# Performance work log

Measured on AMD Instinct MI355X. Metric: run time of the kernel, lower is better.

The kernel has to match this reference:

```python
import jax, jax.numpy as jnp
import numpy as np
from jax import lax

DN = ('NHWC', 'HWIO', 'NHWC')  # conv dimension numbers


def setup_inputs() -> dict:
    key = jax.random.key(0)
    ks = jax.random.split(key, 10)
    B, H, W, C, F, E = 16, 32, 32, 128, 128, 8
    G = F * (H // 2) * (W // 2)  # 32768, gating flatten size
    return {
        'x': jax.random.normal(ks[0], (B, H, W, C), jnp.float32),
        'eps_kernel': jax.random.normal(ks[1], (3, 3, C, F, E), jnp.float32),
        'eps_gate': jax.random.normal(ks[2], (B, E), jnp.float32),
        'expert_mu': jax.random.normal(ks[3], (3, 3, C, F, E), jnp.float32) * 0.05,
        'expert_rho': jax.random.normal(ks[4], (3, C, F, E), jnp.float32) * 0.01 - 6.0,
        'expert_bias': jax.random.normal(ks[5], (F, E), jnp.float32) * 0.01,
        'gating_kernel': jax.random.normal(ks[6], (3, 3, C, F), jnp.float32) * 0.05,
        'gating_bias': jax.random.normal(ks[7], (F,), jnp.float32) * 0.01,
        'gating_out_kernel': jax.random.normal(ks[8], (G, E), jnp.float32) * 0.01,
        'gating_out_bias': jax.random.normal(ks[9], (E,), jnp.float32) * 0.01,
    }


def reference(x, eps_kernel, eps_gate, expert_mu, expert_rho, expert_bias,
              gating_kernel, gating_bias, gating_out_kernel, gating_out_bias):
    GATING_NOISE_SIGMA = 1e-4
    TOP_K = 2
    B = x.shape[0]
    kh, kw, C, F, E = expert_mu.shape

    # Bayesian reparameterized expert kernels: rho shared over first kernel dim
    sigma = jax.nn.softplus(expert_rho)[None]               # [1,kw,C,F,E]
    kernel = expert_mu + sigma * eps_kernel                 # [kh,kw,C,F,E]

    # All-expert conv as one grouped conv via output-channel packing
    kern_flat = kernel.reshape(kh, kw, C, F * E)
    expert_out = lax.conv_general_dilated(x, kern_flat, (1, 1), 'SAME',
                                          dimension_numbers=DN)
    expert_out = expert_out.reshape(B, x.shape[1], x.shape[2], F, E)
    expert_out = expert_out + expert_bias                   # [B,H,W,F,E]

    # Gating path: conv -> 2x2 maxpool -> flatten -> dense -> noisy logits
    g = lax.conv_general_dilated(x, gating_kernel, (1, 1), 'SAME',
                                 dimension_numbers=DN) + gating_bias
    g = lax.reduce_window(g, -jnp.inf, lax.max,
                          (1, 2, 2, 1), (1, 2, 2, 1), 'VALID')
    logits = g.reshape(B, -1) @ gating_out_kernel + gating_out_bias  # [B,E]
    logits = logits + GATING_NOISE_SIGMA * eps_gate

    # noisy top-k gating: softmax over selected experts, zero elsewhere
    top_vals, top_idx = lax.top_k(logits, TOP_K)
    top_w = jax.nn.softmax(top_vals, axis=-1)
    gates = jnp.zeros((B, E), logits.dtype).at[
        jnp.arange(B)[:, None], top_idx].set(top_w)

    # combine experts weighted by gates, broadcast over spatial dims
    out = jnp.einsum('bhwfe,be->bhwf', expert_out, gates)
    return out
```

## Files before the change

### kernel.cpp

```cpp
#include <hip/hip_runtime.h>
#include <cmath>

#define B_ 16
#define H_ 32
#define W_ 32
#define C_ 128
#define F_ 128
#define KSZ (9*C_*F_)
#define NKS 36
#define FRAG_ELE 4096

typedef __bf16 bf16;
typedef __bf16 bf16x4 __attribute__((ext_vector_type(4)));
typedef __bf16 bf16x8 __attribute__((ext_vector_type(8)));
typedef float  f32x4  __attribute__((ext_vector_type(4)));

__device__ __forceinline__ float softplus_f(float v) {
  return log1pf(expf(-fabsf(v))) + fmaxf(v, 0.f);
}

__device__ __forceinline__ float logit_f(const float* part, const float* gob,
                                         const float* epsg, int bb, int e) {
  float s = 0.f;
  #pragma unroll
  for (int hb = 0; hb < 16; ++hb) s += part[(bb*16 + hb)*8 + e];
  return s + gob[e] + 1e-4f * epsg[bb*8 + e];
}

__device__ __forceinline__ void block_map_f(int bid, int* b, int* hb) {
  *b  = (bid & 7) * 2 + (bid >> 7);
  *hb = (bid >> 3) & 15;
}

template<int MODE>
__global__ __launch_bounds__(1024) void conv_k(
    const float* __restrict__ x,
    const bf16* __restrict__ Bhi,
    const bf16* __restrict__ Blo,
    const float* __restrict__ gb,
    const float* __restrict__ Wg,
    const float* __restrict__ part,
    const float* __restrict__ gob,
    const float* __restrict__ epsg,
    const float* __restrict__ ebias,
    const float* __restrict__ mu,
    const float* __restrict__ rho,
    const float* __restrict__ epsk,
    bf16* __restrict__ bank,
    float* __restrict__ outv)
{
  const int t = threadIdx.x;
  const int l = t & 63;

  if (MODE == 2 && blockIdx.x < NKS) {
    if (t < 512) {
      const int ks = blockIdx.x;
      const int nf = t >> 6;
      const int khkw = ks >> 2, kw = khkw % 3;
      const int f  = nf*16 + (l & 15);
      const int cb = (ks & 3)*32 + (l >> 4)*8;
      bf16x8 ob[8];
      #pragma unroll
      for (int j = 0; j < 8; ++j) {
        const int c = cb + j;
        const float* mp = &mu  [(size_t)((khkw*C_ + c)*F_ + f) * 8];
        const float* ep = &epsk[(size_t)((khkw*C_ + c)*F_ + f) * 8];
        const float* rp = &rho [(size_t)((kw  *C_ + c)*F_ + f) * 8];
        #pragma unroll
        for (int e = 0; e < 8; ++e)
          ob[e][j] = (bf16)(mp[e] + softplus_f(rp[e]) * ep[e]);
      }
      #pragma unroll
      for (int e = 0; e < 8; ++e) {
        size_t o = (size_t)e*KSZ + (size_t)ks*FRAG_ELE + nf*512 + l*8;
        *(bf16x8*)&bank[o] = ob[e];
      }
    }
    return;
  }

  int b, hb;
  block_map_f(MODE == 2 ? blockIdx.x - NKS : blockIdx.x, &b, &hb);
  const int wid = t >> 6;
  const int kg  = wid >> 3;
  const int w8  = wid & 7;

  __shared__ bf16 xs[MODE*4*34*128];
  __shared__ float red[8][8];
  __shared__ float gl8[8];
  __shared__ float gw2[2];
  __shared__ int   eid2[2];

  for (int v = t; v < 4*34*32; v += 1024) {
    int c4   = v & 31;
    int col  = (v >> 5) % 34;
    int rowi = (v >> 5) / 34;
    int row  = hb*2 - 1 + rowi;
    int w    = col - 1;
    float4 xv = make_float4(0.f, 0.f, 0.f, 0.f);
    if (row >= 0 && row < H_ && w >= 0 && w < W_)
      xv = *(const float4*)&x[((b*H_ + row)*W_ + w)*C_ + c4*4];
    float vv[4] = {xv.x, xv.y, xv.z, xv.w};
    bf16x4 h4, l4;
    #pragma unroll
    for (int j = 0; j < 4; ++j) {
      h4[j] = (bf16)vv[j];
      if (MODE == 2) l4[j] = (bf16)(vv[j] - (float)h4[j]);
    }
    int base = ((rowi*34 + col)*256 + c4*8) ^ ((col & 7) << 4);
    *(bf16x4*)((char*)xs + base) = h4;
    if (MODE == 2) *(bf16x4*)((char*)xs + 34816 + base) = l4;
  }
  if (MODE == 1 && t == 0) {
    float lg[8];
    #pragma unroll
    for (int e = 0; e < 8; ++e) lg[e] = logit_f(part, gob, epsg, b, e);
    int i0 = 0;
    #pragma unroll
    for (int e = 1; e < 8; ++e) if (lg[e] > lg[i0]) i0 = e;
    int i1 = (i0 == 0) ? 1 : 0;
    #pragma unroll
    for (int e = 0; e < 8; ++e) if (e != i0 && lg[e] > lg[i1]) i1 = e;
    float m  = fmaxf(lg[i0], lg[i1]);
    float e0 = expf(lg[i0] - m), e1 = expf(lg[i1] - m);
    float s  = e0 + e1;
    #pragma unroll
    for (int e = 0; e < 8; ++e) gl8[e] = 0.f;
    gl8[i0] = e0 / s;  gl8[i1] = e1 / s;
    eid2[0] = i0;      eid2[1] = i1;
    gw2[0]  = e0 / s;  gw2[1]  = e1 / s;
  }
  __syncthreads();

  const int mpar = w8 & 1;
  const int nf0  = (w8 >> 1) << 1;
  const int r15  = l & 15;
  const int q    = l >> 4;

  f32x4 acc00 = {0.f,0.f,0.f,0.f}, acc01 = acc00, acc10 = acc00, acc11 = acc00;
  f32x4 acd00 = acc00, acd01 = acc00, acd10 = acc00, acd11 = acc00;

  const bf16* B0;
  const bf16* B1;
  if (MODE == 1) { B0 = Bhi + (size_t)eid2[0]*KSZ; B1 = Bhi + (size_t)eid2[1]*KSZ; }
  else           { B0 = Bhi;                       B1 = Blo; }
  const size_t bgo = (size_t)(nf0*512 + l*8);

  bf16x8 s0h0,s0h1,s0l0,s0l1, s1h0,s1h1,s1l0,s1l1, s2h0,s2h1,s2l0,s2l1;

#define LOADB(S, KS_) do {                                                  \
    int kk_ = (KS_); if (kk_ > NKS-1) kk_ = NKS-1;                          \
    size_t o_ = bgo + (size_t)kk_ * FRAG_ELE;                               \
    S##h0 = *(const bf16x8*)(B0 + o_);                                      \
    S##h1 = *(const bf16x8*)(B0 + o_ + 512);                                \
    S##l0 = *(const bf16x8*)(B1 + o_);                                      \
    S##l1 = *(const bf16x8*)(B1 + o_ + 512);                                \
  } while (0)

#define MFMA16(a, bb_, c) __builtin_amdgcn_mfma_f32_16x16x32_bf16(a, bb_, c, 0, 0, 0)

#define COMPUTE(S, KS_) do {                                                \
    const int khkw_ = (KS_) >> 2;                                           \
    const int kh_ = khkw_ / 3, kw_ = khkw_ % 3;                             \
    const int c0_ = ((KS_) & 3) << 5;                                       \
    const int col_ = mpar*16 + r15 + kw_;                                   \
    const int off_ = ((kh_*34 + col_)*256 + (c0_ + q*8)*2) ^ ((col_ & 7) << 4); \
    bf16x8 a0_ = *(const bf16x8*)((const char*)xs + off_);                  \
    bf16x8 a1_ = *(const bf16x8*)((const char*)xs + off_ + 8704);           \
    __builtin_amdgcn_s_setprio(1);                                          \
    acc00 = MFMA16(a0_, S##h0, acc00);                                      \
    acc01 = MFMA16(a0_, S##h1, acc01);                                      \
    acc10 = MFMA16(a1_, S##h0, acc10);                                      \
    acc11 = MFMA16(a1_, S##h1, acc11);                                      \
    if (MODE == 2) {                                                        \
      bf16x8 g0_ = *(const bf16x8*)((const char*)xs + 34816 + off_);        \
      bf16x8 g1_ = *(const bf16x8*)((const char*)xs + 34816 + off_ + 8704); \
      acc00 = MFMA16(g0_, S##h0, acc00);                                    \
      acc01 = MFMA16(g0_, S##h1, acc01);                                    \
      acc10 = MFMA16(g1_, S##h0, acc10);                                    \
      acc11 = MFMA16(g1_, S##h1, acc11);                                    \
      acc00 = MFMA16(a0_, S##l0, acc00);                                    \
      acc01 = MFMA16(a0_, S##l1, acc01);                                    \
      acc10 = MFMA16(a1_, S##l0, acc10);                                    \
      acc11 = MFMA16(a1_, S##l1, acc11);                                    \
    } else {                                                                \
      acd00 = MFMA16(a0_, S##l0, acd00);                                    \
      acd01 = MFMA16(a0_, S##l1, acd01);                                    \
      acd10 = MFMA16(a1_, S##l0, acd10);                                    \
      acd11 = MFMA16(a1_, S##l1, acd11);                                    \
    }                                                                       \
    __builtin_amdgcn_s_setprio(0);                                          \
  } while (0)

  const int ks0 = kg * (NKS/2);
  LOADB(s0, ks0); LOADB(s1, ks0+1); LOADB(s2, ks0+2);
  for (int ks = ks0; ks < ks0 + NKS/2; ks += 3) {
    COMPUTE(s0, ks);   LOADB(s0, ks+3);
    COMPUTE(s1, ks+1); LOADB(s1, ks+4);
    COMPUTE(s2, ks+2); LOADB(s2, ks+5);
  }
#undef LOADB
#undef COMPUTE

  if (MODE == 1) {
    const float g0 = gw2[0], g1 = gw2[1];
    #pragma unroll
    for (int r = 0; r < 4; ++r) {
      acc00[r] = g0*acc00[r] + g1*acd00[r];
      acc01[r] = g0*acc01[r] + g1*acd01[r];
      acc10[r] = g0*acc10[r] + g1*acd10[r];
      acc11[r] = g0*acc11[r] + g1*acd11[r];
    }
  }

  __syncthreads();
  float* comb = (float*)xs;
  if (kg == 1) {
    #pragma unroll
    for (int r = 0; r < 4; ++r) {
      comb[(w8*16 + 0  + r)*64 + l] = acc00[r];
      comb[(w8*16 + 4  + r)*64 + l] = acc01[r];
      comb[(w8*16 + 8  + r)*64 + l] = acc10[r];
      comb[(w8*16 + 12 + r)*64 + l] = acc11[r];
    }
  }
  __syncthreads();
  if (kg == 0) {
    #pragma unroll
    for (int r = 0; r < 4; ++r) {
      acc00[r] += comb[(w8*16 + 0  + r)*64 + l];
      acc01[r] += comb[(w8*16 + 4  + r)*64 + l];
      acc10[r] += comb[(w8*16 + 8  + r)*64 + l];
      acc11[r] += comb[(w8*16 + 12 + r)*64 + l];
    }
  }

  if (MODE == 1) {
    if (kg == 0) {
      const int f0 = nf0*16 + r15;
      float bv0 = 0.f, bv1 = 0.f;
      #pragma unroll
      for (int e = 0; e < 8; ++e) {
        bv0 += gl8[e] * ebias[f0*8 + e];
        bv1 += gl8[e] * ebias[(f0+16)*8 + e];
      }
      #pragma unroll
      for (int mi = 0; mi < 2; ++mi) {
        const int h = hb*2 + mi;
        #pragma unroll
        for (int r = 0; r < 4; ++r) {
          const int wo = mpar*16 + q*4 + r;
          float* o = &outv[((b*H_ + h)*W_ + wo)*F_];
          o[f0]      = (mi ? acc10[r] : acc00[r]) + bv0;
          o[f0 + 16] = (mi ? acc11[r] : acc01[r]) + bv1;
        }
      }
    }
  } else {
    float pr[8] = {0,0,0,0,0,0,0,0};
    if (kg == 0) {
      #pragma unroll
      for (int ni = 0; ni < 2; ++ni) {
        const int f = (nf0 + ni)*16 + r15;
        const float bv = gb[f];
        #pragma unroll
        for (int pp = 0; pp < 2; ++pp) {
          float m0 = ni ? fmaxf(acc01[2*pp], acc01[2*pp+1])
                        : fmaxf(acc00[2*pp], acc00[2*pp+1]);
          float m1 = ni ? fmaxf(acc11[2*pp], acc11[2*pp+1])
                        : fmaxf(acc10[2*pp], acc10[2*pp+1]);
          float pm = fmaxf(m0, m1) + bv;
          const int pw = mpar*8 + q*2 + pp;
          const float* wr = &Wg[(size_t)((hb*16 + pw)*128 + f) * 8];
          float4 wA = *(const float4*)wr;
          float4 wB = *(const float4*)(wr + 4);
          pr[0] += pm*wA.x; pr[1] += pm*wA.y; pr[2] += pm*wA.z; pr[3] += pm*wA.w;
          pr[4] += pm*wB.x; pr[5] += pm*wB.y; pr[6] += pm*wB.z; pr[7] += pm*wB.w;
        }
      }
    }
    #pragma unroll
    for (int o = 32; o > 0; o >>= 1)
      #pragma unroll
      for (int e = 0; e < 8; ++e) pr[e] += __shfl_down(pr[e], o);
    if (l == 0 && kg == 0)
      #pragma unroll
      for (int e = 0; e < 8; ++e) red[w8][e] = pr[e];
    __syncthreads();
    if (t < 8) {
      float s = 0.f;
      #pragma unroll
      for (int w = 0; w < 8; ++w) s += red[w][t];
      outv[(b*16 + hb)*8 + t] = s;
    }
  }
}

__global__ __launch_bounds__(1024) void gkprep_k(
    const float* __restrict__ gk, bf16* __restrict__ bgh, bf16* __restrict__ bgl)
{
  __shared__ float tile[32*129];
  const int ks   = blockIdx.x;
  const int khkw = ks >> 2;
  const int cb   = (ks & 3)*32;
  const int t    = threadIdx.x;

  {
    int c  = t >> 5;
    int f4 = (t & 31) * 4;
    float4 val = *(const float4*)&gk[(size_t)(khkw*C_ + cb + c)*F_ + f4];
    float* dst = &tile[c*129 + f4];
    dst[0] = val.x; dst[1] = val.y; dst[2] = val.z; dst[3] = val.w;
  }
  __syncthreads();

  if (t < 512) {
    const int nf = t >> 6, l = t & 63;
    const int f  = nf*16 + (l & 15);
    bf16x8 h8, l8;
    #pragma unroll
    for (int j = 0; j < 8; ++j) {
      int c = (l >> 4)*8 + j;
      float v = tile[c*129 + f];
      bf16 h = (bf16)v;
      h8[j] = h;
      l8[j] = (bf16)(v - (float)h);
    }
    *(bf16x8*)&bgh[(size_t)ks*FRAG_ELE + t*8] = h8;
    *(bf16x8*)&bgl[(size_t)ks*FRAG_ELE + t*8] = l8;
  }
}

extern "C" void kernel_launch(void* const* d_in, const int* in_sizes, int n_in,
                              void* d_out, int out_size, void* d_ws, size_t ws_size,
                              hipStream_t stream) {
  const float* x    = (const float*)d_in[0];
  const float* epsk = (const float*)d_in[1];
  const float* epsg = (const float*)d_in[2];
  const float* mu   = (const float*)d_in[3];
  const float* rho  = (const float*)d_in[4];
  const float* ebias= (const float*)d_in[5];
  const float* gk   = (const float*)d_in[6];
  const float* gb   = (const float*)d_in[7];
  const float* gok  = (const float*)d_in[8];
  const float* gob  = (const float*)d_in[9];
  float* out = (float*)d_out;

  char* ws = (char*)d_ws;
  bf16*  bank = (bf16*) (ws);
  bf16*  bgh  = (bf16*) (ws + 2359296);
  bf16*  bgl  = (bf16*) (ws + 2654208);
  float* part = (float*)(ws + 2949120);

  gkprep_k<<<NKS, 1024, 0, stream>>>(gk, bgh, bgl);
  conv_k<2><<<NKS + 256, 1024, 0, stream>>>(x, bgh, bgl, gb, gok,
                                            nullptr, nullptr, nullptr, nullptr,
                                            mu, rho, epsk, bank, part);
  conv_k<1><<<256, 1024, 0, stream>>>(x, bank, nullptr, nullptr, nullptr,
                                      part, gob, epsg, ebias,
                                      nullptr, nullptr, nullptr, nullptr, out);
}
```

Measured before the change: 55.03 us.

## Pre-pad and pre-convert input to bf16 hi/lo, stage via global_load_lds

```diff
diff --git a/kernel.cpp b/kernel.cpp
--- a/kernel.cpp
+++ b/kernel.cpp
@@ -9,6 +9,7 @@
 #define KSZ (9*C_*F_)
 #define NKS 36
 #define FRAG_ELE 4096
+#define XPB (34*34*128)
 
 typedef __bf16 bf16;
 typedef __bf16 bf16x4 __attribute__((ext_vector_type(4)));
@@ -34,7 +35,7 @@
 
 template<int MODE>
 __global__ __launch_bounds__(1024) void conv_k(
-    const float* __restrict__ x,
+    const bf16* __restrict__ xpadh, const bf16* __restrict__ xpadl,
     const bf16* __restrict__ Bhi,
     const bf16* __restrict__ Blo,
     const float* __restrict__ gb,
@@ -91,26 +92,6 @@
   __shared__ float gw2[2];
   __shared__ int   eid2[2];
 
-  for (int v = t; v < 4*34*32; v += 1024) {
-    int c4   = v & 31;
-    int col  = (v >> 5) % 34;
-    int rowi = (v >> 5) / 34;
-    int row  = hb*2 - 1 + rowi;
-    int w    = col - 1;
-    float4 xv = make_float4(0.f, 0.f, 0.f, 0.f);
-    if (row >= 0 && row < H_ && w >= 0 && w < W_)
-      xv = *(const float4*)&x[((b*H_ + row)*W_ + w)*C_ + c4*4];
-    float vv[4] = {xv.x, xv.y, xv.z, xv.w};
-    bf16x4 h4, l4;
-    #pragma unroll
-    for (int j = 0; j < 4; ++j) {
-      h4[j] = (bf16)vv[j];
-      if (MODE == 2) l4[j] = (bf16)(vv[j] - (float)h4[j]);
-    }
-    int base = ((rowi*34 + col)*256 + c4*8) ^ ((col & 7) << 4);
-    *(bf16x4*)((char*)xs + base) = h4;
-    if (MODE == 2) *(bf16x4*)((char*)xs + 34816 + base) = l4;
-  }
   if (MODE == 1 && t == 0) {
     float lg[8];
     #pragma unroll
@@ -129,6 +110,26 @@
     gl8[i0] = e0 / s;  gl8[i1] = e1 / s;
     eid2[0] = i0;      eid2[1] = i1;
     gw2[0]  = e0 / s;  gw2[1]  = e1 / s;
+  }
+
+  {
+    const size_t bb = (size_t)b * XPB;
+    const int rowbase = hb * 2;
+    for (int dd = wid; dd < 34*MODE; dd += 16) {
+      const int variant = (MODE == 2 && dd >= 34) ? 1 : 0;
+      const int d = dd - 34*variant;
+      const int L = d*4 + (l >> 4);
+      const int rowi = L / 34;
+      const int col  = L % 34;
+      const int srcoff = ((l & 15)*16) ^ ((col & 7) << 4);
+      const bf16* src = (variant ? xpadl : xpadh) + bb
+                        + ((size_t)(rowbase + rowi)*34 + col)*128
+                        + (srcoff >> 1);
+      bf16* dst = &xs[variant*(4*34*128) + d*512];
+      __builtin_amdgcn_global_load_lds(
+          (const __attribute__((address_space(1))) void*)src,
+          (__attribute__((address_space(3))) void*)dst, 16, 0, 0);
+    }
   }
   __syncthreads();
 
@@ -167,7 +168,6 @@
     const int off_ = ((kh_*34 + col_)*256 + (c0_ + q*8)*2) ^ ((col_ & 7) << 4); \
     bf16x8 a0_ = *(const bf16x8*)((const char*)xs + off_);                  \
     bf16x8 a1_ = *(const bf16x8*)((const char*)xs + off_ + 8704);           \
-    __builtin_amdgcn_s_setprio(1);                                          \
     acc00 = MFMA16(a0_, S##h0, acc00);                                      \
     acc01 = MFMA16(a0_, S##h1, acc01);                                      \
     acc10 = MFMA16(a1_, S##h0, acc10);                                      \
@@ -189,7 +189,6 @@
       acd10 = MFMA16(a1_, S##l0, acd10);                                    \
       acd11 = MFMA16(a1_, S##l1, acd11);                                    \
     }                                                                       \
-    __builtin_amdgcn_s_setprio(0);                                          \
   } while (0)
 
   const int ks0 = kg * (NKS/2);
@@ -296,38 +295,56 @@
   }
 }
 
-__global__ __launch_bounds__(1024) void gkprep_k(
-    const float* __restrict__ gk, bf16* __restrict__ bgh, bf16* __restrict__ bgl)
+__global__ __launch_bounds__(1024) void prep_k(
+    const float* __restrict__ gk, const float* __restrict__ x,
+    bf16* __restrict__ bgh, bf16* __restrict__ bgl,
+    bf16* __restrict__ xpadh, bf16* __restrict__ xpadl)
 {
-  __shared__ float tile[32*129];
-  const int ks   = blockIdx.x;
-  const int khkw = ks >> 2;
-  const int cb   = (ks & 3)*32;
-  const int t    = threadIdx.x;
-
-  {
-    int c  = t >> 5;
-    int f4 = (t & 31) * 4;
-    float4 val = *(const float4*)&gk[(size_t)(khkw*C_ + cb + c)*F_ + f4];
-    float* dst = &tile[c*129 + f4];
-    dst[0] = val.x; dst[1] = val.y; dst[2] = val.z; dst[3] = val.w;
-  }
-  __syncthreads();
-
-  if (t < 512) {
-    const int nf = t >> 6, l = t & 63;
-    const int f  = nf*16 + (l & 15);
-    bf16x8 h8, l8;
-    #pragma unroll
-    for (int j = 0; j < 8; ++j) {
-      int c = (l >> 4)*8 + j;
-      float v = tile[c*129 + f];
+  const int t = threadIdx.x;
+  if (blockIdx.x < NKS) {
+    __shared__ float tile[32*129];
+    const int ks   = blockIdx.x;
+    const int khkw = ks >> 2;
+    const int cb   = (ks & 3)*32;
+    {
+      int c  = t >> 5;
+      int f4 = (t & 31) * 4;
+      float4 val = *(const float4*)&gk[(size_t)(khkw*C_ + cb + c)*F_ + f4];
+      float* dst = &tile[c*129 + f4];
+      dst[0] = val.x; dst[1] = val.y; dst[2] = val.z; dst[3] = val.w;
+    }
+    __syncthreads();
+    if (t < 512) {
+      const int nf = t >> 6, l = t & 63;
+      const int f  = nf*16 + (l & 15);
+      bf16x8 h8, l8;
+      #pragma unroll
+      for (int j = 0; j < 8; ++j) {
+        int c = (l >> 4)*8 + j;
+        float v = tile[c*129 + f];
+        bf16 h = (bf16)v;
+        h8[j] = h;
+        l8[j] = (bf16)(v - (float)h);
+      }
+      *(bf16x8*)&bgh[(size_t)ks*FRAG_ELE + t*8] = h8;
+      *(bf16x8*)&bgl[(size_t)ks*FRAG_ELE + t*8] = l8;
+    }
+  } else {
+    const int idx = blockIdx.x - NKS;
+    const int b = idx / 34;
+    const int p = idx % 34;
+    const size_t base = (size_t)b*XPB + (size_t)p*34*128;
+    const bool rowin = (p >= 1 && p <= 32);
+    for (int e = t; e < 34*128; e += 1024) {
+      const int colp = e >> 7;
+      const int c    = e & 127;
+      float v = 0.f;
+      if (rowin && colp >= 1 && colp <= 32)
+        v = x[(((size_t)b*H_ + (p-1))*W_ + (colp-1))*C_ + c];
       bf16 h = (bf16)v;
-      h8[j] = h;
-      l8[j] = (bf16)(v - (float)h);
-    }
-    *(bf16x8*)&bgh[(size_t)ks*FRAG_ELE + t*8] = h8;
-    *(bf16x8*)&bgl[(size_t)ks*FRAG_ELE + t*8] = l8;
+      xpadh[base + e] = h;
+      xpadl[base + e] = (bf16)(v - (float)h);
+    }
   }
 }
 
@@ -347,16 +364,19 @@
   float* out = (float*)d_out;
 
   char* ws = (char*)d_ws;
-  bf16*  bank = (bf16*) (ws);
-  bf16*  bgh  = (bf16*) (ws + 2359296);
-  bf16*  bgl  = (bf16*) (ws + 2654208);
-  float* part = (float*)(ws + 2949120);
-
-  gkprep_k<<<NKS, 1024, 0, stream>>>(gk, bgh, bgl);
-  conv_k<2><<<NKS + 256, 1024, 0, stream>>>(x, bgh, bgl, gb, gok,
+  bf16*  bank  = (bf16*) (ws);
+  bf16*  bgh   = (bf16*) (ws + 2359296);
+  bf16*  bgl   = (bf16*) (ws + 2654208);
+  bf16*  xpadh = (bf16*) (ws + 2949120);
+  bf16*  xpadl = (bf16*) (ws + 7684096);
+  float* part  = (float*)(ws + 12419072);
+
+  prep_k<<<NKS + B_*34, 1024, 0, stream>>>(gk, x, bgh, bgl, xpadh, xpadl);
+  conv_k<2><<<NKS + 256, 1024, 0, stream>>>(xpadh, xpadl, bgh, bgl, gb, gok,
                                             nullptr, nullptr, nullptr, nullptr,
                                             mu, rho, epsk, bank, part);
-  conv_k<1><<<256, 1024, 0, stream>>>(x, bank, nullptr, nullptr, nullptr,
+  conv_k<1><<<256, 1024, 0, stream>>>(xpadh, xpadh, bank, nullptr,
+                                      nullptr, nullptr,
                                       part, gob, epsg, ebias,
                                       nullptr, nullptr, nullptr, nullptr, out);
 }
```

Measured after the change: 58.07 us. 1.06x slower.
